# Kernel tuning notes

Hardware: AMD Instinct MI355X
Metric: run time of the kernel (lower is better)

Reference implementation:

```python
import jax, jax.numpy as jnp
import numpy as np

N_ATOMS = 32768
N_EDGES = 262144
ATOM_F = 256
EDGE_F = 128
OUT_F = 512
N_GAUSS = 50
SPIN_D = 3


def setup_inputs() -> dict:
    key = jax.random.key(0)
    k1, k2, k3, k4, k5 = jax.random.split(key, 5)
    h = jax.random.normal(k1, (N_ATOMS, ATOM_F), dtype=jnp.float32)
    m = jax.random.normal(k2, (N_EDGES, EDGE_F), dtype=jnp.float32)
    magft_cat = jax.random.normal(k3, (N_ATOMS, SPIN_D), dtype=jnp.float32)
    edge_index = jax.random.randint(k4, (2, N_EDGES), 0, N_ATOMS, dtype=jnp.int64)
    in_f = 2 * ATOM_F + EDGE_F + N_GAUSS  # 690
    W = jax.random.normal(k5, (OUT_F, in_f), dtype=jnp.float32) * 0.02
    return {"h": h, "m": m, "magft_cat": magft_cat, "edge_index": edge_index, "W": W}


def reference(h, m, magft_cat, edge_index, W):
    # GaussianSmearing(-1.5, 1.5, 50)
    offsets = jnp.linspace(-1.5, 1.5, N_GAUSS, dtype=jnp.float32)  # (G,)
    coeff = -0.5 / (offsets[1] - offsets[0]) ** 2

    src = edge_index[0]
    tgt = edge_index[1]
    h_s = h[src]                     # (E, A)
    h_t = h[tgt]                     # (E, A)
    # per-edge spin dot product, (E, 1)
    d = jnp.sum(magft_cat[src] * magft_cat[tgt], axis=1, keepdims=True)
    spin_edge = jnp.exp(coeff * (d - offsets) ** 2)  # (E, G)
    m_st = jnp.concatenate([h_s, h_t, m, spin_edge], axis=-1)  # (E, 690)
    # bias-free Dense with activation=None
    return m_st @ W.T  # (E, OUT_F)
```

## Files before the change

### kernel.cpp

```cpp
#include <hip/hip_runtime.h>
#include <hip/hip_bf16.h>

#define N_ATOMS 32768
#define N_EDGESC 262144
#define ATOM_F 256
#define EDGE_F 128
#define OUT_F 512
#define N_GAUSS 50
#define IN_F 690
#define NCHUNK 11

#define BM 128
#define BN 256
#define NTHREADS 512

using f32x4  = __attribute__((ext_vector_type(4))) float;
using short8 = __attribute__((ext_vector_type(8))) short;

__device__ __forceinline__ unsigned short f2bf(float f) {
  unsigned int u = __builtin_bit_cast(unsigned int, f);
  u += 0x7fffu + ((u >> 16) & 1u);
  return (unsigned short)(u >> 16);
}

__global__ void detect_idx_kernel(const unsigned int* __restrict__ ei, int* __restrict__ flag) {
  if (threadIdx.x == 0) {
    int ok = 1;
    for (int i = 0; i < 64; ++i) {
      unsigned int lo = ei[2 * i], hi = ei[2 * i + 1];
      if (hi != 0u || lo >= (unsigned)N_ATOMS) { ok = 0; break; }
    }
    *flag = ok;
  }
}

__global__ void prep_h_kernel(const float* __restrict__ h, unsigned short* __restrict__ hb) {
  size_t i = (size_t)(blockIdx.x * blockDim.x + threadIdx.x) * 8;
  if (i >= (size_t)N_ATOMS * ATOM_F) return;
  float4 a = *(const float4*)(h + i);
  float4 b = *(const float4*)(h + i + 4);
  uint4 o;
  o.x = (unsigned)f2bf(a.x) | ((unsigned)f2bf(a.y) << 16);
  o.y = (unsigned)f2bf(a.z) | ((unsigned)f2bf(a.w) << 16);
  o.z = (unsigned)f2bf(b.x) | ((unsigned)f2bf(b.y) << 16);
  o.w = (unsigned)f2bf(b.z) | ((unsigned)f2bf(b.w) << 16);
  *(uint4*)(hb + i) = o;
}

__global__ void prep_w_kernel(const float* __restrict__ W, unsigned short* __restrict__ Wp) {
  int g = blockIdx.x * blockDim.x + threadIdx.x;
  if (g >= NCHUNK * 2 * 32 * 64) return;
  int l  = g & 63;
  int nt = (g >> 6) & 31;
  int ks = (g >> 11) & 1;
  int kc = g >> 12;
  int n  = nt * 16 + (l & 15);
  int k0 = kc * 64 + ks * 32 + ((l >> 4) << 3);
  unsigned int u[4];
#pragma unroll
  for (int p = 0; p < 4; ++p) {
    int ka = k0 + 2 * p, kb = k0 + 2 * p + 1;
    float va = (ka < IN_F) ? W[n * IN_F + ka] : 0.0f;
    float vb = (kb < IN_F) ? W[n * IN_F + kb] : 0.0f;
    u[p] = (unsigned)f2bf(va) | ((unsigned)f2bf(vb) << 16);
  }
  *(uint4*)(Wp + (size_t)g * 8) = make_uint4(u[0], u[1], u[2], u[3]);
}

__global__ __launch_bounds__(NTHREADS, 4) void gemm_kernel(
    const unsigned short* __restrict__ hb, const float* __restrict__ m,
    const float* __restrict__ magft, const void* __restrict__ ei,
    const int* __restrict__ flagp, const unsigned short* __restrict__ Wp,
    float* __restrict__ out)
{
  __shared__ __align__(16) unsigned short As[3][BM * 64];
  __shared__ int sIdx[BM], tIdx[BM];
  __shared__ float dLDS[BM];

  const int tid = threadIdx.x;
  const int bid = blockIdx.x;
  const int e  = (bid & 7) | ((bid >> 4) << 3);
  const int nh = (bid >> 3) & 1;
  const int eb = e * BM;

  const int use64 = *flagp;
  if (tid < BM) {
    int ed = eb + tid;
    int s, tg;
    if (use64) {
      const long long* p = (const long long*)ei;
      s  = (int)p[ed];
      tg = (int)p[N_EDGESC + ed];
    } else {
      const int* p = (const int*)ei;
      s  = p[ed];
      tg = p[N_EDGESC + ed];
    }
    sIdx[tid] = s;
    tIdx[tid] = tg;
    float ax = magft[3 * s],  ay = magft[3 * s + 1],  az = magft[3 * s + 2];
    float bx = magft[3 * tg], by = magft[3 * tg + 1], bz = magft[3 * tg + 2];
    dLDS[tid] = ax * bx + ay * by + az * bz;
  }
  __syncthreads();

  const int lane = tid & 63;
  const int wid  = tid >> 6;
  const int wr   = wid >> 2;
  const int wc   = wid & 3;

  const int r0 = wid * 16 + (lane >> 3);
  const int hs0 = sIdx[r0], hs1 = sIdx[r0 + 8];
  const int ht0 = tIdx[r0], ht1 = tIdx[r0 + 8];
  const int srcsw = (((lane & 7) ^ (lane >> 3)) << 4);

  const int ar = tid >> 2;
  const int aq = tid & 3;

  auto stage = [&](int kchunk, int buf) {
    if (kchunk < 8) {
      int a0 = (kchunk < 4) ? hs0 : ht0;
      int a1 = (kchunk < 4) ? hs1 : ht1;
      const unsigned short* s0 = hb + (size_t)a0 * ATOM_F + (kchunk & 3) * 64;
      const unsigned short* s1 = hb + (size_t)a1 * ATOM_F + (kchunk & 3) * 64;
      char* d0 = (char*)&As[buf][0] + wid * 2048;
      __builtin_amdgcn_global_load_lds(
          (const __attribute__((address_space(1))) void*)((const char*)s0 + srcsw),
          (__attribute__((address_space(3))) void*)d0, 16, 0, 0);
      __builtin_amdgcn_global_load_lds(
          (const __attribute__((address_space(1))) void*)((const char*)s1 + srcsw),
          (__attribute__((address_space(3))) void*)(d0 + 1024), 16, 0, 0);
    } else if (kchunk < 10) {
      const float* p = m + (size_t)(eb + ar) * EDGE_F + (kchunk & 1) * 64 + aq * 16;
      char* base = (char*)&As[buf][0] + ar * 128;
      const int sw = (ar & 7) << 4;
#pragma unroll
      for (int hh = 0; hh < 2; ++hh) {
        float4 v0 = ((const float4*)p)[2 * hh];
        float4 v1 = ((const float4*)p)[2 * hh + 1];
        uint4 o;
        o.x = (unsigned)f2bf(v0.x) | ((unsigned)f2bf(v0.y) << 16);
        o.y = (unsigned)f2bf(v0.z) | ((unsigned)f2bf(v0.w) << 16);
        o.z = (unsigned)f2bf(v1.x) | ((unsigned)f2bf(v1.y) << 16);
        o.w = (unsigned)f2bf(v1.z) | ((unsigned)f2bf(v1.w) << 16);
        *(uint4*)(base + ((aq * 32 + hh * 16) ^ sw)) = o;
      }
    } else {
      float d = dLDS[ar];
      const float step  = 3.0f / 49.0f;
      const float coeff = -0.5f / (step * step);
      char* base = (char*)&As[buf][0] + ar * 128;
      const int sw = (ar & 7) << 4;
#pragma unroll
      for (int hh = 0; hh < 2; ++hh) {
        unsigned int u[4];
#pragma unroll
        for (int p2 = 0; p2 < 4; ++p2) {
          int c0 = aq * 16 + hh * 8 + 2 * p2, c1 = c0 + 1;
          float o0 = -1.5f + step * (float)c0;
          float o1 = -1.5f + step * (float)c1;
          float w0 = (c0 < N_GAUSS) ? __expf(coeff * (d - o0) * (d - o0)) : 0.0f;
          float w1 = (c1 < N_GAUSS) ? __expf(coeff * (d - o1) * (d - o1)) : 0.0f;
          u[p2] = (unsigned)f2bf(w0) | ((unsigned)f2bf(w1) << 16);
        }
        *(uint4*)(base + ((aq * 32 + hh * 16) ^ sw)) = make_uint4(u[0], u[1], u[2], u[3]);
      }
    }
  };

  f32x4 acc[4][4];
#pragma unroll
  for (int i = 0; i < 4; ++i)
#pragma unroll
    for (int j = 0; j < 4; ++j) acc[i][j] = (f32x4){0.f, 0.f, 0.f, 0.f};

  const short8* Wp8 = (const short8*)Wp;

  auto compute = [&](int kc, int buf) {
    const char* abase = (const char*)&As[buf][0];
#pragma unroll
    for (int ks = 0; ks < 2; ++ks) {
      short8 b[4];
#pragma unroll
      for (int ni = 0; ni < 4; ++ni) {
        int nt = nh * 16 + wc * 4 + ni;
        b[ni] = Wp8[(size_t)(((kc * 2 + ks) * 32 + nt) << 6) + lane];
      }
      short8 a[4];
#pragma unroll
      for (int mi = 0; mi < 4; ++mi) {
        int row = wr * 64 + mi * 16 + (lane & 15);
        int colb = (ks * 64 + ((lane >> 4) << 4)) ^ ((row & 7) << 4);
        a[mi] = *(const short8*)(abase + row * 128 + colb);
      }
      __builtin_amdgcn_s_setprio(1);
#pragma unroll
      for (int mi = 0; mi < 4; ++mi)
#pragma unroll
        for (int ni = 0; ni < 4; ++ni)
          acc[mi][ni] = __builtin_amdgcn_mfma_f32_16x16x32_bf16(a[mi], b[ni], acc[mi][ni], 0, 0, 0);
      __builtin_amdgcn_s_setprio(0);
    }
  };

  stage(0, 0);
  stage(1, 1);
  __syncthreads();

  for (int kc = 0; kc < 6; ++kc) {
    stage(kc + 2, (kc + 2) % 3);
    compute(kc, kc % 3);
    asm volatile("s_waitcnt vmcnt(2) lgkmcnt(0)" ::: "memory");
    __builtin_amdgcn_sched_barrier(0);
    __builtin_amdgcn_s_barrier();
  }
  for (int kc = 6; kc < NCHUNK; ++kc) {
    if (kc + 2 < NCHUNK) stage(kc + 2, (kc + 2) % 3);
    compute(kc, kc % 3);
    if (kc + 1 < NCHUNK) {
      asm volatile("s_waitcnt vmcnt(0) lgkmcnt(0)" ::: "memory");
      __builtin_amdgcn_sched_barrier(0);
      __builtin_amdgcn_s_barrier();
    }
  }

#pragma unroll
  for (int mi = 0; mi < 4; ++mi) {
    int row0 = eb + wr * 64 + mi * 16 + ((lane >> 4) << 2);
#pragma unroll
    for (int ni = 0; ni < 4; ++ni) {
      int col = nh * 256 + wc * 64 + ni * 16 + (lane & 15);
#pragma unroll
      for (int j = 0; j < 4; ++j) {
        out[(size_t)(row0 + j) * OUT_F + col] = acc[mi][ni][j];
      }
    }
  }
}

extern "C" void kernel_launch(void* const* d_in, const int* in_sizes, int n_in,
                              void* d_out, int out_size, void* d_ws, size_t ws_size,
                              hipStream_t stream) {
  const float* h     = (const float*)d_in[0];
  const float* m     = (const float*)d_in[1];
  const float* magft = (const float*)d_in[2];
  const void*  ei    = d_in[3];
  const float* W     = (const float*)d_in[4];
  float* out = (float*)d_out;

  char* ws = (char*)d_ws;
  int* flag = (int*)ws;
  unsigned short* Wp = (unsigned short*)(ws + 256);
  unsigned short* hb = (unsigned short*)(ws + 256 + 720896);

  detect_idx_kernel<<<1, 64, 0, stream>>>((const unsigned int*)ei, flag);
  prep_w_kernel<<<(NCHUNK * 2 * 32 * 64 + 255) / 256, 256, 0, stream>>>(W, Wp);
  prep_h_kernel<<<(N_ATOMS * ATOM_F / 8 + 255) / 256, 256, 0, stream>>>(h, hb);

  gemm_kernel<<<dim3(2 * N_EDGESC / BM), NTHREADS, 0, stream>>>(hb, m, magft, ei, flag, Wp, out);
}
```

Baseline: 294.1 us.

## Switch GEMM to 32x32x16 bf16 MFMA with rotated k-step order

Replaces the 16x16x32 MFMA tiling (4x4 tiles per wave) with 32x32x16 MFMA (2x2 tiles per wave). The weight prepack layout, the A-fragment LDS reads and the output store mapping all change to match. Each wave also starts its four k-substeps at a wave-dependent offset, which is meant to spread LDS bank and weight-load traffic across waves. The larger MFMA needs fewer instructions and fewer operand fetches per FLOP. In exchange, each wave's output stores now cover 32 columns with a stride-8 row pattern.

```diff
diff --git a/kernel.cpp b/kernel.cpp
--- a/kernel.cpp
+++ b/kernel.cpp
@@ -14,7 +14,7 @@
 #define BN 256
 #define NTHREADS 512
 
-using f32x4  = __attribute__((ext_vector_type(4))) float;
+using f32x16 = __attribute__((ext_vector_type(16))) float;
 using short8 = __attribute__((ext_vector_type(8))) short;
 
 __device__ __forceinline__ unsigned short f2bf(float f) {
@@ -49,13 +49,13 @@
 
 __global__ void prep_w_kernel(const float* __restrict__ W, unsigned short* __restrict__ Wp) {
   int g = blockIdx.x * blockDim.x + threadIdx.x;
-  if (g >= NCHUNK * 2 * 32 * 64) return;
+  if (g >= NCHUNK * 4 * 16 * 64) return;
   int l  = g & 63;
-  int nt = (g >> 6) & 31;
-  int ks = (g >> 11) & 1;
+  int nt = (g >> 6) & 15;
+  int kk = (g >> 10) & 3;
   int kc = g >> 12;
-  int n  = nt * 16 + (l & 15);
-  int k0 = kc * 64 + ks * 32 + ((l >> 4) << 3);
+  int n  = nt * 32 + (l & 31);
+  int k0 = kc * 64 + kk * 16 + ((l >> 5) << 3);
   unsigned int u[4];
 #pragma unroll
   for (int p = 0; p < 4; ++p) {
@@ -168,37 +168,38 @@
     }
   };
 
-  f32x4 acc[4][4];
-#pragma unroll
-  for (int i = 0; i < 4; ++i)
-#pragma unroll
-    for (int j = 0; j < 4; ++j) acc[i][j] = (f32x4){0.f, 0.f, 0.f, 0.f};
+  f32x16 acc[2][2];
+#pragma unroll
+  for (int i = 0; i < 2; ++i)
+#pragma unroll
+    for (int j = 0; j < 2; ++j)
+#pragma unroll
+      for (int r = 0; r < 16; ++r) acc[i][j][r] = 0.f;
 
   const short8* Wp8 = (const short8*)Wp;
 
   auto compute = [&](int kc, int buf) {
     const char* abase = (const char*)&As[buf][0];
 #pragma unroll
-    for (int ks = 0; ks < 2; ++ks) {
-      short8 b[4];
-#pragma unroll
-      for (int ni = 0; ni < 4; ++ni) {
-        int nt = nh * 16 + wc * 4 + ni;
-        b[ni] = Wp8[(size_t)(((kc * 2 + ks) * 32 + nt) << 6) + lane];
-      }
-      short8 a[4];
-#pragma unroll
-      for (int mi = 0; mi < 4; ++mi) {
-        int row = wr * 64 + mi * 16 + (lane & 15);
-        int colb = (ks * 64 + ((lane >> 4) << 4)) ^ ((row & 7) << 4);
+    for (int t = 0; t < 4; ++t) {
+      const int kk = (t + wid) & 3;
+      short8 b[2];
+#pragma unroll
+      for (int ni = 0; ni < 2; ++ni)
+        b[ni] = Wp8[(size_t)((((kc * 4 + kk) * 16) + nh * 8 + wc * 2 + ni) << 6) + lane];
+      short8 a[2];
+#pragma unroll
+      for (int mi = 0; mi < 2; ++mi) {
+        int row = wr * 64 + mi * 32 + (lane & 31);
+        int colb = (kk * 32 + ((lane >> 5) << 4)) ^ ((row & 7) << 4);
         a[mi] = *(const short8*)(abase + row * 128 + colb);
       }
       __builtin_amdgcn_s_setprio(1);
 #pragma unroll
-      for (int mi = 0; mi < 4; ++mi)
-#pragma unroll
-        for (int ni = 0; ni < 4; ++ni)
-          acc[mi][ni] = __builtin_amdgcn_mfma_f32_16x16x32_bf16(a[mi], b[ni], acc[mi][ni], 0, 0, 0);
+      for (int mi = 0; mi < 2; ++mi)
+#pragma unroll
+        for (int ni = 0; ni < 2; ++ni)
+          acc[mi][ni] = __builtin_amdgcn_mfma_f32_32x32x16_bf16(a[mi], b[ni], acc[mi][ni], 0, 0, 0);
       __builtin_amdgcn_s_setprio(0);
     }
   };
@@ -225,14 +226,15 @@
   }
 
 #pragma unroll
-  for (int mi = 0; mi < 4; ++mi) {
-    int row0 = eb + wr * 64 + mi * 16 + ((lane >> 4) << 2);
-#pragma unroll
-    for (int ni = 0; ni < 4; ++ni) {
-      int col = nh * 256 + wc * 64 + ni * 16 + (lane & 15);
-#pragma unroll
-      for (int j = 0; j < 4; ++j) {
-        out[(size_t)(row0 + j) * OUT_F + col] = acc[mi][ni][j];
+  for (int mi = 0; mi < 2; ++mi) {
+#pragma unroll
+    for (int ni = 0; ni < 2; ++ni) {
+      int col = nh * 256 + wc * 64 + ni * 32 + (lane & 31);
+      int rbase = eb + wr * 64 + mi * 32 + ((lane >> 5) << 2);
+#pragma unroll
+      for (int r = 0; r < 16; ++r) {
+        int row = rbase + (r & 3) + ((r >> 2) << 3);
+        out[(size_t)row * OUT_F + col] = acc[mi][ni][r];
       }
     }
   }
@@ -254,7 +256,7 @@
   unsigned short* hb = (unsigned short*)(ws + 256 + 720896);
 
   detect_idx_kernel<<<1, 64, 0, stream>>>((const unsigned int*)ei, flag);
-  prep_w_kernel<<<(NCHUNK * 2 * 32 * 64 + 255) / 256, 256, 0, stream>>>(W, Wp);
+  prep_w_kernel<<<(NCHUNK * 4 * 16 * 64 + 255) / 256, 256, 0, stream>>>(W, Wp);
   prep_h_kernel<<<(N_ATOMS * ATOM_F / 8 + 255) / 256, 256, 0, stream>>>(h, hb);
 
   gemm_kernel<<<dim3(2 * N_EDGESC / BM), NTHREADS, 0, stream>>>(hb, m, magft, ei, flag, Wp, out);
```

Result: slower. 317.8 us (+8.1%).

## Reorder K-chunks to stage register-path chunks first and deepen async gather pipeline

Applied to the files above, without the earlier changes.

The K loop is reordered so the m and Gaussian chunks, which go through registers, are staged up front, and only the async global_load_lds h-gather chunks run through the pipelined loop. The LDS ring grows from 3 to 4 buffers, so three gathers can be in flight (vmcnt(4)). The goal is to keep register-path conversion work out of the steady-state loop and hide more gather latency. The extra 16KB of LDS per block may cut occupancy below the 4 blocks per CU requested by launch bounds.

```diff
diff --git a/kernel.cpp b/kernel.cpp
--- a/kernel.cpp
+++ b/kernel.cpp
@@ -73,7 +73,7 @@
     const int* __restrict__ flagp, const unsigned short* __restrict__ Wp,
     float* __restrict__ out)
 {
-  __shared__ __align__(16) unsigned short As[3][BM * 64];
+  __shared__ __align__(16) unsigned short As[4][BM * 64];
   __shared__ int sIdx[BM], tIdx[BM];
   __shared__ float dLDS[BM];
 
@@ -117,23 +117,25 @@
   const int ar = tid >> 2;
   const int aq = tid & 3;
 
-  auto stage = [&](int kchunk, int buf) {
-    if (kchunk < 8) {
-      int a0 = (kchunk < 4) ? hs0 : ht0;
-      int a1 = (kchunk < 4) ? hs1 : ht1;
-      const unsigned short* s0 = hb + (size_t)a0 * ATOM_F + (kchunk & 3) * 64;
-      const unsigned short* s1 = hb + (size_t)a1 * ATOM_F + (kchunk & 3) * 64;
-      char* d0 = (char*)&As[buf][0] + wid * 2048;
-      __builtin_amdgcn_global_load_lds(
-          (const __attribute__((address_space(1))) void*)((const char*)s0 + srcsw),
-          (__attribute__((address_space(3))) void*)d0, 16, 0, 0);
-      __builtin_amdgcn_global_load_lds(
-          (const __attribute__((address_space(1))) void*)((const char*)s1 + srcsw),
-          (__attribute__((address_space(3))) void*)(d0 + 1024), 16, 0, 0);
-    } else if (kchunk < 10) {
+  auto stage_h = [&](int kchunk, int buf) {
+    int a0 = (kchunk < 4) ? hs0 : ht0;
+    int a1 = (kchunk < 4) ? hs1 : ht1;
+    const unsigned short* s0 = hb + (size_t)a0 * ATOM_F + (kchunk & 3) * 64;
+    const unsigned short* s1 = hb + (size_t)a1 * ATOM_F + (kchunk & 3) * 64;
+    char* d0 = (char*)&As[buf][0] + wid * 2048;
+    __builtin_amdgcn_global_load_lds(
+        (const __attribute__((address_space(1))) void*)((const char*)s0 + srcsw),
+        (__attribute__((address_space(3))) void*)d0, 16, 0, 0);
+    __builtin_amdgcn_global_load_lds(
+        (const __attribute__((address_space(1))) void*)((const char*)s1 + srcsw),
+        (__attribute__((address_space(3))) void*)(d0 + 1024), 16, 0, 0);
+  };
+
+  auto stage_reg = [&](int kchunk, int buf) {
+    char* base = (char*)&As[buf][0] + ar * 128;
+    const int sw = (ar & 7) << 4;
+    if (kchunk < 10) {
       const float* p = m + (size_t)(eb + ar) * EDGE_F + (kchunk & 1) * 64 + aq * 16;
-      char* base = (char*)&As[buf][0] + ar * 128;
-      const int sw = (ar & 7) << 4;
 #pragma unroll
       for (int hh = 0; hh < 2; ++hh) {
         float4 v0 = ((const float4*)p)[2 * hh];
@@ -149,8 +151,6 @@
       float d = dLDS[ar];
       const float step  = 3.0f / 49.0f;
       const float coeff = -0.5f / (step * step);
-      char* base = (char*)&As[buf][0] + ar * 128;
-      const int sw = (ar & 7) << 4;
 #pragma unroll
       for (int hh = 0; hh < 2; ++hh) {
         unsigned int u[4];
@@ -203,26 +203,28 @@
     }
   };
 
-  stage(0, 0);
-  stage(1, 1);
+  stage_reg(8, 0);
+  stage_reg(9, 1);
+  stage_reg(10, 2);
   __syncthreads();
 
-  for (int kc = 0; kc < 6; ++kc) {
-    stage(kc + 2, (kc + 2) % 3);
-    compute(kc, kc % 3);
-    asm volatile("s_waitcnt vmcnt(2) lgkmcnt(0)" ::: "memory");
+  for (int pos = 0; pos < 8; ++pos) {
+    stage_h(pos, (pos + 3) & 3);
+    int kc = (pos < 3) ? pos + 8 : pos - 3;
+    compute(kc, pos & 3);
+    asm volatile("s_waitcnt vmcnt(4) lgkmcnt(0)" ::: "memory");
     __builtin_amdgcn_sched_barrier(0);
     __builtin_amdgcn_s_barrier();
   }
-  for (int kc = 6; kc < NCHUNK; ++kc) {
-    if (kc + 2 < NCHUNK) stage(kc + 2, (kc + 2) % 3);
-    compute(kc, kc % 3);
-    if (kc + 1 < NCHUNK) {
-      asm volatile("s_waitcnt vmcnt(0) lgkmcnt(0)" ::: "memory");
-      __builtin_amdgcn_sched_barrier(0);
-      __builtin_amdgcn_s_barrier();
-    }
-  }
+  compute(5, 0);
+  asm volatile("s_waitcnt vmcnt(2) lgkmcnt(0)" ::: "memory");
+  __builtin_amdgcn_sched_barrier(0);
+  __builtin_amdgcn_s_barrier();
+  compute(6, 1);
+  asm volatile("s_waitcnt vmcnt(0) lgkmcnt(0)" ::: "memory");
+  __builtin_amdgcn_sched_barrier(0);
+  __builtin_amdgcn_s_barrier();
+  compute(7, 2);
 
 #pragma unroll
   for (int mi = 0; mi < 4; ++mi) {
```

Result: faster. 279.5 us (-4.9%).
